# Performance work log

Hardware: AMD Instinct MI355X
Metric: run time of the kernel (lower is better)

The kernel has to match this reference:

```python
import jax, jax.numpy as jnp
import numpy as np

NUM_HEADS = 16

def _split_heads(x, H):
    B, S, D = x.shape
    return x.reshape(B, S, H, D // H).transpose(0, 2, 1, 3)  # [B,H,S,hd]

def _merge_heads(x):
    B, H, S, hd = x.shape
    return x.transpose(0, 2, 1, 3).reshape(B, S, H * hd)

def setup_inputs() -> dict:
    key = jax.random.key(0)
    k1, k2, k3, k4 = jax.random.split(key, 4)
    B, S, D = 2, 2048, 1024
    return {
        "visual_features": jax.random.normal(k1, (B, S, D), dtype=jnp.float32),
        "transaction_features": jax.random.normal(k2, (B, S, D), dtype=jnp.float32),
        "W_qkv": jax.random.normal(k3, (D, 3 * D), dtype=jnp.float32) * (1.0 / np.sqrt(D)),
        "W_out": jax.random.normal(k4, (D, D), dtype=jnp.float32) * (1.0 / np.sqrt(D)),
    }

def reference(visual_features, transaction_features, W_qkv, W_out):
    H = NUM_HEADS
    D = visual_features.shape[-1]
    scale = (D // H) ** -0.5

    v_q, v_k, v_v = [_split_heads(t, H) for t in jnp.split(visual_features @ W_qkv, 3, axis=-1)]
    t_q, t_k, t_v = [_split_heads(t, H) for t in jnp.split(transaction_features @ W_qkv, 3, axis=-1)]

    # visual queries attend to transaction keys/values (dropout = identity at eval)
    v2t = jax.nn.softmax(jnp.einsum('bhqd,bhkd->bhqk', v_q, t_k) * scale, axis=-1)
    t2v = jax.nn.softmax(jnp.einsum('bhqd,bhkd->bhqk', t_q, v_k) * scale, axis=-1)

    v2t_out = _merge_heads(jnp.einsum('bhqk,bhkd->bhqd', v2t, t_v))
    t2v_out = _merge_heads(jnp.einsum('bhqk,bhkd->bhqd', t2v, v_v))

    return (v2t_out + t2v_out) @ W_out
```

## Files before the change

kernel.cpp:

```cpp
#include <hip/hip_runtime.h>


typedef short  frag8 __attribute__((ext_vector_type(8)));
typedef float  f32x4 __attribute__((ext_vector_type(4)));

union F8 { frag8 f; uint2 u2[2]; unsigned u[4]; };

#define MFMA16(a,b,c) __builtin_amdgcn_mfma_f32_16x16x32_bf16((a),(b),(c),0,0,0)

__device__ __forceinline__ unsigned short f2bf(float f) {
  unsigned u = __builtin_bit_cast(unsigned, f);
  return (unsigned short)((u + 0x7fffu + ((u >> 16) & 1u)) >> 16);
}
__device__ __forceinline__ float bf2f(unsigned short s) {
  unsigned u = ((unsigned)s) << 16;
  return __builtin_bit_cast(float, u);
}
__device__ __forceinline__ unsigned pkbf(float lo, float hi) {
  unsigned r;
  asm("v_cvt_pk_bf16_f32 %0, %1, %2" : "=v"(r) : "v"(lo), "v"(hi));
  return r;
}

__global__ __launch_bounds__(256) void k_prep(
    const float* __restrict__ vis, const float* __restrict__ trn,
    const float* __restrict__ Wqkv, const float* __restrict__ Wout,
    unsigned short* __restrict__ Abf, unsigned short* __restrict__ Wqb,
    unsigned short* __restrict__ Wob)
{
  size_t i8 = ((size_t)blockIdx.x * 256 + threadIdx.x) * 8;
  const float* src;
  unsigned short* dst;
  if (i8 < 8388608) {
    src = (i8 < 4194304) ? vis + i8 : trn + (i8 - 4194304);
    dst = Abf + i8;
  } else if (i8 < 11534336) {
    size_t o = i8 - 8388608;  src = Wqkv + o; dst = Wqb + o;
  } else {
    size_t o = i8 - 11534336; src = Wout + o; dst = Wob + o;
  }
  float4 u = *(const float4*)src;
  float4 v = *(const float4*)(src + 4);
  uint4 w;
  w.x = pkbf(u.x, u.y); w.y = pkbf(u.z, u.w);
  w.z = pkbf(v.x, v.y); w.w = pkbf(v.z, v.w);
  *(uint4*)dst = w;
}

__global__ __launch_bounds__(256) void k_gemm_qkv_b(
    const unsigned short* __restrict__ Abf, const unsigned short* __restrict__ Wqb,
    unsigned short* __restrict__ qkv)
{
  __shared__ unsigned short As_[128 * 32];
  __shared__ unsigned short Bs[128 * 40];
  const int tid  = threadIdx.x;
  const int lane = tid & 63, wv = tid >> 6;
  const int lm = lane & 15, lg = lane >> 4;
  const int nt = blockIdx.x, mt = blockIdx.y;
  const int wr = (wv >> 1) * 64, wc = (wv & 1) * 64;

  f32x4 acc[4][4] = {};

  const unsigned short* agp =
      Abf + (size_t)(mt * 128 + wv * 32 + (lane >> 2)) * 1024 + (lane & 3) * 8;
  const int bn = (tid & 63) * 2, bk = (tid >> 6) * 8;

  for (int kt = 0; kt < 32; ++kt) {
    __syncthreads();
    {
      __builtin_amdgcn_global_load_lds(
          (const __attribute__((address_space(1))) void*)(agp + kt * 32),
          (__attribute__((address_space(3))) void*)&As_[wv * 1024], 16, 0, 0);
      __builtin_amdgcn_global_load_lds(
          (const __attribute__((address_space(1))) void*)(agp + 16 * 1024 + kt * 32),
          (__attribute__((address_space(3))) void*)&As_[wv * 1024 + 512], 16, 0, 0);
    }
    {
      const unsigned short* bp = Wqb + (size_t)(kt * 32 + bk) * 3072 + nt * 128 + bn;
      frag8 q0, q1;
#pragma unroll
      for (int i = 0; i < 8; ++i) {
        ushort2 t = *(const ushort2*)(bp + (size_t)i * 3072);
        q0[i] = (short)t.x; q1[i] = (short)t.y;
      }
      *(frag8*)&Bs[(bn)     * 40 + bk] = q0;
      *(frag8*)&Bs[(bn + 1) * 40 + bk] = q1;
    }
    __syncthreads();
    frag8 af[4], bfr[4];
#pragma unroll
    for (int mi = 0; mi < 4; ++mi)
      af[mi] = *(const frag8*)&As_[(wr + mi * 16 + lm) * 32 + lg * 8];
#pragma unroll
    for (int ni = 0; ni < 4; ++ni)
      bfr[ni] = *(const frag8*)&Bs[(wc + ni * 16 + lm) * 40 + lg * 8];
#pragma unroll
    for (int mi = 0; mi < 4; ++mi)
#pragma unroll
      for (int ni = 0; ni < 4; ++ni)
        acc[mi][ni] = MFMA16(af[mi], bfr[ni], acc[mi][ni]);
  }

#pragma unroll
  for (int mi = 0; mi < 4; ++mi)
#pragma unroll
    for (int ni = 0; ni < 4; ++ni)
#pragma unroll
      for (int r = 0; r < 4; ++r) {
        int row = mt * 128 + wr + mi * 16 + lg * 4 + r;
        int col = nt * 128 + wc + ni * 16 + lm;
        qkv[(size_t)row * 3072 + col] = f2bf(acc[mi][ni][r]);
      }
}

__global__ __launch_bounds__(256) void k_vt(
    const unsigned short* __restrict__ qkv, unsigned short* __restrict__ Vt)
{
  __shared__ unsigned short L[64 * 72];
  const int tid = threadIdx.x;
  const int sblk = blockIdx.x;
  const int by = blockIdx.y;
  const int src = by >> 4, h = by & 15;
  {
    int sl = tid >> 2, dc = tid & 3;
    const unsigned short* gp =
        qkv + (size_t)(src * 2048 + sblk * 64 + sl) * 3072 + 2048 + h * 64 + dc * 16;
    *(frag8*)&L[sl * 72 + dc * 16]     = *(const frag8*)gp;
    *(frag8*)&L[sl * 72 + dc * 16 + 8] = *(const frag8*)(gp + 8);
  }
  __syncthreads();
  int d = tid >> 2, sc = tid & 3;
  unsigned wbuf[8];
#pragma unroll
  for (int j = 0; j < 8; ++j) {
    unsigned lo = L[(sc * 16 + 2 * j)     * 72 + d];
    unsigned hi = L[(sc * 16 + 2 * j + 1) * 72 + d];
    wbuf[j] = lo | (hi << 16);
  }
  unsigned short* op =
      Vt + ((size_t)(src * 16 + h) * 64 + d) * 2048 + sblk * 64 + sc * 16;
  *(uint4*)op       = *(uint4*)&wbuf[0];
  *(uint4*)(op + 8) = *(uint4*)&wbuf[4];
}

__global__ __launch_bounds__(256) void k_attn(
    const unsigned short* __restrict__ qkv, const unsigned short* __restrict__ Vt,
    unsigned short* __restrict__ Opart, float* __restrict__ lpart)
{
  __shared__ unsigned short Ks[2][32 * 72];
  __shared__ unsigned short Vs[2][8 * 272];
  const int tid  = threadIdx.x;
  const int lane = tid & 63, wv = tid >> 6;
  const int lm = lane & 15, lg = lane >> 4;
  const int qt = blockIdx.x, comb = blockIdx.y;
  const int dir = comb >> 5, bb = (comb >> 4) & 1, h = comb & 15;
  const int half = blockIdx.z;
  const int NT = 32, kt0 = half * 32;
  const int qbase  = (dir ? 4096 : 0) + bb * 2048;
  const int kvbase = (dir ? 0 : 4096) + bb * 2048;
  const int qcol = h * 64, kcol = 1024 + h * 64;

  const float QS = 0.125f * 1.44269504f;
  frag8 qf[2][2];
#pragma unroll
  for (int mi = 0; mi < 2; ++mi)
#pragma unroll
    for (int kb = 0; kb < 2; ++kb) {
      frag8 t = *(const frag8*)&qkv[
          (size_t)(qbase + qt * 128 + wv * 32 + mi * 16 + lm) * 3072 +
          qcol + kb * 32 + lg * 8];
#pragma unroll
      for (int j = 0; j < 8; ++j)
        t[j] = (short)f2bf(bf2f((unsigned short)t[j]) * QS);
      qf[mi][kb] = t;
    }

  f32x4 acc[2][4] = {};
  float lr[2] = {0.0f, 0.0f};

  const int skv = tid >> 3, sd = (tid & 7) * 8;
  const int vd = tid >> 2, vc = tid & 3;
  const unsigned short* __restrict__ kp =
      qkv + (size_t)(kvbase + skv) * 3072 + kcol + sd;
  const unsigned short* __restrict__ vtp =
      Vt + ((size_t)((kvbase >> 11) * 16 + h) * 64 + vd) * 2048 + vc * 8;

  frag8 Rk, Rv;

#define LOAD_R(kt_) do {                                                   \
    Rk = *(const frag8*)(kp + (size_t)(kt_) * (32 * 3072));                \
    Rv = *(const frag8*)(vtp + (size_t)(kt_) * 32);                        \
  } while (0)

#define WRITE_R(s_) do {                                                   \
    *(frag8*)&Ks[s_][skv * 72 + sd] = Rk;                                  \
    F8 tv_; tv_.f = Rv;                                                    \
    *(uint2*)&Vs[s_][(2 * vc) * 272 + vd * 4]     = tv_.u2[0];             \
    *(uint2*)&Vs[s_][(2 * vc + 1) * 272 + vd * 4] = tv_.u2[1];             \
  } while (0)

  LOAD_R(kt0);
  WRITE_R(0);
  LOAD_R(kt0 + 1);

  for (int i = 0; i < NT; ++i) {
    __syncthreads();
    if (i < NT - 1) WRITE_R((i + 1) & 1);
    if (i < NT - 2) LOAD_R(kt0 + i + 2);
    const int s = i & 1;

    frag8 kf[2][2];
#pragma unroll
    for (int t = 0; t < 2; ++t)
#pragma unroll
      for (int kb = 0; kb < 2; ++kb)
        kf[t][kb] = *(const frag8*)&Ks[s][(t * 16 + lm) * 72 + kb * 32 + lg * 8];
    f32x4 st[2][2] = {};
#pragma unroll
    for (int mi = 0; mi < 2; ++mi)
#pragma unroll
      for (int t = 0; t < 2; ++t)
#pragma unroll
        for (int kb = 0; kb < 2; ++kb)
          st[mi][t] = MFMA16(kf[t][kb], qf[mi][kb], st[mi][t]);

    frag8 pa[2];
#pragma unroll
    for (int mi = 0; mi < 2; ++mi) {
      f32x4 a = st[mi][0], b = st[mi][1];
      float p[8];
#pragma unroll
      for (int r = 0; r < 4; ++r) p[r]     = exp2f(a[r]);
#pragma unroll
      for (int r = 0; r < 4; ++r) p[4 + r] = exp2f(b[r]);
      lr[mi] += ((p[0] + p[1]) + (p[2] + p[3])) +
                ((p[4] + p[5]) + (p[6] + p[7]));
      F8 pk_;
      pk_.u[0] = pkbf(p[0], p[1]); pk_.u[1] = pkbf(p[2], p[3]);
      pk_.u[2] = pkbf(p[4], p[5]); pk_.u[3] = pkbf(p[6], p[7]);
      pa[mi] = pk_.f;
    }

    frag8 vb[4];
#pragma unroll
    for (int di = 0; di < 4; ++di) {
      F8 t;
      t.u2[0] = *(const uint2*)&Vs[s][lg * 272 + (di * 16 + lm) * 4];
      t.u2[1] = *(const uint2*)&Vs[s][(4 + lg) * 272 + (di * 16 + lm) * 4];
      vb[di] = t.f;
    }
#pragma unroll
    for (int mi = 0; mi < 2; ++mi)
#pragma unroll
      for (int di = 0; di < 4; ++di)
        acc[mi][di] = MFMA16(pa[mi], vb[di], acc[mi][di]);
  }

#undef LOAD_R
#undef WRITE_R

#pragma unroll
  for (int mi = 0; mi < 2; ++mi) {
    float l = lr[mi];
    l += __shfl_xor(l, 16);
    l += __shfl_xor(l, 32);
    int rowb = bb * 2048 + qt * 128 + wv * 32 + mi * 16;
    if (lane < 16)
      lpart[(size_t)(half * 2 + dir) * 65536 + h * 4096 + rowb + lane] = l;
#pragma unroll
    for (int r = 0; r < 4; ++r) {
      int row = rowb + lg * 4 + r;
#pragma unroll
      for (int di = 0; di < 4; ++di) {
        int col = h * 64 + di * 16 + lm;
        Opart[((size_t)(half * 2 + dir) * 4096 + row) * 1024 + col] =
            f2bf(acc[mi][di][r]);
      }
    }
  }
}

__global__ __launch_bounds__(256) void k_combine(
    const unsigned short* __restrict__ Op, const float* __restrict__ lp,
    unsigned short* __restrict__ a0, unsigned short* __restrict__ a1)
{
  int g   = blockIdx.x * 256 + threadIdx.x;
  int col = (g & 255) << 2;
  int row = (g >> 8) & 4095;
  int dir = g >> 20;
  int h   = col >> 6;
  float l = lp[(size_t)dir * 65536 + h * 4096 + row] +
            lp[(size_t)(2 + dir) * 65536 + h * 4096 + row];
  float inv = 1.0f / l;
  const unsigned short* pu = &Op[((size_t)dir * 4096 + row) * 1024 + col];
  const unsigned short* pv = &Op[((size_t)(2 + dir) * 4096 + row) * 1024 + col];
  uint2 w;
  w.x = pkbf((bf2f(pu[0]) + bf2f(pv[0])) * inv, (bf2f(pu[1]) + bf2f(pv[1])) * inv);
  w.y = pkbf((bf2f(pu[2]) + bf2f(pv[2])) * inv, (bf2f(pu[3]) + bf2f(pv[3])) * inv);
  unsigned short* dst = dir ? a1 : a0;
  *(uint2*)&dst[(size_t)row * 1024 + col] = w;
}

__global__ __launch_bounds__(256) void k_gemm_out_b(
    const unsigned short* __restrict__ x0, const unsigned short* __restrict__ x1,
    const unsigned short* __restrict__ Wob, float* __restrict__ out)
{
  __shared__ unsigned short As[128 * 40];
  __shared__ unsigned short Bs[128 * 40];
  const int tid  = threadIdx.x;
  const int lane = tid & 63, wv = tid >> 6;
  const int lm = lane & 15, lg = lane >> 4;
  const int nt = blockIdx.x, mt = blockIdx.y;
  const int wr = (wv >> 1) * 64, wc = (wv & 1) * 64;

  f32x4 acc[4][4] = {};

  const int am = tid >> 1, akq = (tid & 1) * 16;
  const int arow = mt * 128 + am;
  const unsigned short* __restrict__ a0p = x0 + (size_t)arow * 1024;
  const unsigned short* __restrict__ a1p = x1 + (size_t)arow * 1024;
  const int bn = (tid & 63) * 2, bk = (tid >> 6) * 8;

  for (int kt = 0; kt < 32; ++kt) {
    __syncthreads();
    {
      frag8 u0 = *(const frag8*)(a0p + kt * 32 + akq);
      frag8 u1 = *(const frag8*)(a0p + kt * 32 + akq + 8);
      frag8 w0 = *(const frag8*)(a1p + kt * 32 + akq);
      frag8 w1 = *(const frag8*)(a1p + kt * 32 + akq + 8);
      frag8 p0, p1;
#pragma unroll
      for (int j = 0; j < 8; ++j) {
        p0[j] = (short)f2bf(bf2f((unsigned short)u0[j]) + bf2f((unsigned short)w0[j]));
        p1[j] = (short)f2bf(bf2f((unsigned short)u1[j]) + bf2f((unsigned short)w1[j]));
      }
      *(frag8*)&As[am * 40 + akq]     = p0;
      *(frag8*)&As[am * 40 + akq + 8] = p1;
    }
    {
      const unsigned short* bp = Wob + (size_t)(kt * 32 + bk) * 1024 + nt * 128 + bn;
      frag8 q0, q1;
#pragma unroll
      for (int i = 0; i < 8; ++i) {
        ushort2 t = *(const ushort2*)(bp + (size_t)i * 1024);
        q0[i] = (short)t.x; q1[i] = (short)t.y;
      }
      *(frag8*)&Bs[(bn)     * 40 + bk] = q0;
      *(frag8*)&Bs[(bn + 1) * 40 + bk] = q1;
    }
    __syncthreads();
    frag8 af[4], bfr[4];
#pragma unroll
    for (int mi = 0; mi < 4; ++mi)
      af[mi] = *(const frag8*)&As[(wr + mi * 16 + lm) * 40 + lg * 8];
#pragma unroll
    for (int ni = 0; ni < 4; ++ni)
      bfr[ni] = *(const frag8*)&Bs[(wc + ni * 16 + lm) * 40 + lg * 8];
#pragma unroll
    for (int mi = 0; mi < 4; ++mi)
#pragma unroll
      for (int ni = 0; ni < 4; ++ni)
        acc[mi][ni] = MFMA16(af[mi], bfr[ni], acc[mi][ni]);
  }

#pragma unroll
  for (int mi = 0; mi < 4; ++mi)
#pragma unroll
    for (int ni = 0; ni < 4; ++ni)
#pragma unroll
      for (int r = 0; r < 4; ++r) {
        int row = mt * 128 + wr + mi * 16 + lg * 4 + r;
        int col = nt * 128 + wc + ni * 16 + lm;
        out[(size_t)row * 1024 + col] = acc[mi][ni][r];
      }
}

extern "C" void kernel_launch(void* const* d_in, const int* in_sizes, int n_in,
                              void* d_out, int out_size, void* d_ws, size_t ws_size,
                              hipStream_t stream)
{
  const float* vis  = (const float*)d_in[0];
  const float* trn  = (const float*)d_in[1];
  const float* Wqkv = (const float*)d_in[2];
  const float* Wout = (const float*)d_in[3];
  float* out = (float*)d_out;

  char* base = (char*)d_ws;
  unsigned short* qkv = (unsigned short*)base;
  unsigned short* a0  = (unsigned short*)(base + 50331648UL);
  unsigned short* a1  = a0 + 4194304;
  unsigned short* Vt  = (unsigned short*)(base + 67108864UL);
  unsigned short* Wob = (unsigned short*)(base + 83886080UL);
  float*          lp  = (float*)(base + 85983232UL);
  unsigned short* Abf = (unsigned short*)(base + 87031808UL);
  unsigned short* Wqb = Abf + 8388608;
  unsigned short* Op  = (unsigned short*)(base + 87031808UL);

  k_prep     <<<6144, 256, 0, stream>>>(vis, trn, Wqkv, Wout, Abf, Wqb, Wob);
  k_gemm_qkv_b<<<dim3(24, 64), 256, 0, stream>>>(Abf, Wqb, qkv);
  k_vt       <<<dim3(32, 64), 256, 0, stream>>>(qkv, Vt);
  k_attn     <<<dim3(16, 64, 2), 256, 0, stream>>>(qkv, Vt, Op, lp);
  k_combine  <<<8192, 256, 0, stream>>>(Op, lp, a0, a1);
  k_gemm_out_b<<<dim3(8, 32), 256, 0, stream>>>(a0, a1, Wob, out);
}
```

Before: 268.4 us.

## Pre-transpose weights to N-major bf16 and stream B tiles via global_load_lds

Adds a k_wt kernel that converts W_qkv and W_out to bf16 and transposes them to [N][K] layout through shared memory. Both GEMMs can then load B tiles with direct global-to-LDS 16-byte loads instead of strided 2-element gathers and register transposes. The softmax exp2f calls are also replaced with raw v_exp_f32 inline asm, which skips the library's range handling. The cost is two extra small launches per call, and the exp change relies on inputs staying in the range the hardware instruction handles.

Result: faster. 243.7 us (-9.2%).

```diff
diff --git a/kernel.cpp b/kernel.cpp
--- a/kernel.cpp
+++ b/kernel.cpp
@@ -21,38 +21,63 @@
   asm("v_cvt_pk_bf16_f32 %0, %1, %2" : "=v"(r) : "v"(lo), "v"(hi));
   return r;
 }
+__device__ __forceinline__ float fexp2(float x) {
+  float r;
+  asm("v_exp_f32 %0, %1" : "=v"(r) : "v"(x));
+  return r;
+}
 
 __global__ __launch_bounds__(256) void k_prep(
     const float* __restrict__ vis, const float* __restrict__ trn,
-    const float* __restrict__ Wqkv, const float* __restrict__ Wout,
-    unsigned short* __restrict__ Abf, unsigned short* __restrict__ Wqb,
-    unsigned short* __restrict__ Wob)
+    unsigned short* __restrict__ Abf)
 {
   size_t i8 = ((size_t)blockIdx.x * 256 + threadIdx.x) * 8;
-  const float* src;
-  unsigned short* dst;
-  if (i8 < 8388608) {
-    src = (i8 < 4194304) ? vis + i8 : trn + (i8 - 4194304);
-    dst = Abf + i8;
-  } else if (i8 < 11534336) {
-    size_t o = i8 - 8388608;  src = Wqkv + o; dst = Wqb + o;
-  } else {
-    size_t o = i8 - 11534336; src = Wout + o; dst = Wob + o;
-  }
+  const float* src = (i8 < 4194304) ? vis + i8 : trn + (i8 - 4194304);
   float4 u = *(const float4*)src;
   float4 v = *(const float4*)(src + 4);
   uint4 w;
   w.x = pkbf(u.x, u.y); w.y = pkbf(u.z, u.w);
   w.z = pkbf(v.x, v.y); w.w = pkbf(v.z, v.w);
-  *(uint4*)dst = w;
+  *(uint4*)(Abf + i8) = w;
+}
+
+__global__ __launch_bounds__(256) void k_wt(
+    const float* __restrict__ W, unsigned short* __restrict__ Wt, int N)
+{
+  __shared__ unsigned short L[64 * 72];
+  const int tid = threadIdx.x;
+  const int n0 = blockIdx.x * 64, k0 = blockIdx.y * 64;
+  {
+    int kr = tid >> 2, c4 = (tid & 3) * 16;
+    const float* gp = W + (size_t)(k0 + kr) * N + n0 + c4;
+    float4 u0 = *(const float4*)gp,       u1 = *(const float4*)(gp + 4);
+    float4 u2 = *(const float4*)(gp + 8), u3 = *(const float4*)(gp + 12);
+    unsigned* lw = (unsigned*)&L[kr * 72 + c4];
+    lw[0] = pkbf(u0.x, u0.y); lw[1] = pkbf(u0.z, u0.w);
+    lw[2] = pkbf(u1.x, u1.y); lw[3] = pkbf(u1.z, u1.w);
+    lw[4] = pkbf(u2.x, u2.y); lw[5] = pkbf(u2.z, u2.w);
+    lw[6] = pkbf(u3.x, u3.y); lw[7] = pkbf(u3.z, u3.w);
+  }
+  __syncthreads();
+  int nr = tid >> 2, kc = (tid & 3) * 16;
+  unsigned wb[8];
+#pragma unroll
+  for (int j = 0; j < 8; ++j) {
+    unsigned lo = L[(kc + 2 * j)     * 72 + nr];
+    unsigned hi = L[(kc + 2 * j + 1) * 72 + nr];
+    wb[j] = lo | (hi << 16);
+  }
+  unsigned short* op = Wt + (size_t)(n0 + nr) * 1024 + k0 + kc;
+  *(uint4*)op       = *(uint4*)&wb[0];
+  *(uint4*)(op + 8) = *(uint4*)&wb[4];
 }
 
 __global__ __launch_bounds__(256) void k_gemm_qkv_b(
-    const unsigned short* __restrict__ Abf, const unsigned short* __restrict__ Wqb,
+    const unsigned short* __restrict__ Abf, const unsigned short* __restrict__ WqbT,
     unsigned short* __restrict__ qkv)
 {
   __shared__ unsigned short As_[128 * 32];
-  __shared__ unsigned short Bs[128 * 40];
+  __shared__ unsigned short Bs_[128 * 32];
   const int tid  = threadIdx.x;
   const int lane = tid & 63, wv = tid >> 6;
   const int lm = lane & 15, lg = lane >> 4;
@@ -63,29 +88,23 @@
 
   const unsigned short* agp =
       Abf + (size_t)(mt * 128 + wv * 32 + (lane >> 2)) * 1024 + (lane & 3) * 8;
-  const int bn = (tid & 63) * 2, bk = (tid >> 6) * 8;
+  const unsigned short* bgp =
+      WqbT + (size_t)(nt * 128 + wv * 32 + (lane >> 2)) * 1024 + (lane & 3) * 8;
 
   for (int kt = 0; kt < 32; ++kt) {
     __syncthreads();
-    {
-      __builtin_amdgcn_global_load_lds(
-          (const __attribute__((address_space(1))) void*)(agp + kt * 32),
-          (__attribute__((address_space(3))) void*)&As_[wv * 1024], 16, 0, 0);
-      __builtin_amdgcn_global_load_lds(
-          (const __attribute__((address_space(1))) void*)(agp + 16 * 1024 + kt * 32),
-          (__attribute__((address_space(3))) void*)&As_[wv * 1024 + 512], 16, 0, 0);
-    }
-    {
-      const unsigned short* bp = Wqb + (size_t)(kt * 32 + bk) * 3072 + nt * 128 + bn;
-      frag8 q0, q1;
-#pragma unroll
-      for (int i = 0; i < 8; ++i) {
-        ushort2 t = *(const ushort2*)(bp + (size_t)i * 3072);
-        q0[i] = (short)t.x; q1[i] = (short)t.y;
-      }
-      *(frag8*)&Bs[(bn)     * 40 + bk] = q0;
-      *(frag8*)&Bs[(bn + 1) * 40 + bk] = q1;
-    }
+    __builtin_amdgcn_global_load_lds(
+        (const __attribute__((address_space(1))) void*)(agp + kt * 32),
+        (__attribute__((address_space(3))) void*)&As_[wv * 1024], 16, 0, 0);
+    __builtin_amdgcn_global_load_lds(
+        (const __attribute__((address_space(1))) void*)(agp + 16 * 1024 + kt * 32),
+        (__attribute__((address_space(3))) void*)&As_[wv * 1024 + 512], 16, 0, 0);
+    __builtin_amdgcn_global_load_lds(
+        (const __attribute__((address_space(1))) void*)(bgp + kt * 32),
+        (__attribute__((address_space(3))) void*)&Bs_[wv * 1024], 16, 0, 0);
+    __builtin_amdgcn_global_load_lds(
+        (const __attribute__((address_space(1))) void*)(bgp + 16 * 1024 + kt * 32),
+        (__attribute__((address_space(3))) void*)&Bs_[wv * 1024 + 512], 16, 0, 0);
     __syncthreads();
     frag8 af[4], bfr[4];
 #pragma unroll
@@ -93,7 +112,7 @@
       af[mi] = *(const frag8*)&As_[(wr + mi * 16 + lm) * 32 + lg * 8];
 #pragma unroll
     for (int ni = 0; ni < 4; ++ni)
-      bfr[ni] = *(const frag8*)&Bs[(wc + ni * 16 + lm) * 40 + lg * 8];
+      bfr[ni] = *(const frag8*)&Bs_[(wc + ni * 16 + lm) * 32 + lg * 8];
 #pragma unroll
     for (int mi = 0; mi < 4; ++mi)
 #pragma unroll
@@ -230,9 +249,9 @@
       f32x4 a = st[mi][0], b = st[mi][1];
       float p[8];
 #pragma unroll
-      for (int r = 0; r < 4; ++r) p[r]     = exp2f(a[r]);
-#pragma unroll
-      for (int r = 0; r < 4; ++r) p[4 + r] = exp2f(b[r]);
+      for (int r = 0; r < 4; ++r) p[r]     = fexp2(a[r]);
+#pragma unroll
+      for (int r = 0; r < 4; ++r) p[4 + r] = fexp2(b[r]);
       lr[mi] += ((p[0] + p[1]) + (p[2] + p[3])) +
                 ((p[4] + p[5]) + (p[6] + p[7]));
       F8 pk_;
@@ -303,10 +322,10 @@
 
 __global__ __launch_bounds__(256) void k_gemm_out_b(
     const unsigned short* __restrict__ x0, const unsigned short* __restrict__ x1,
-    const unsigned short* __restrict__ Wob, float* __restrict__ out)
+    const unsigned short* __restrict__ WobT, float* __restrict__ out)
 {
   __shared__ unsigned short As[128 * 40];
-  __shared__ unsigned short Bs[128 * 40];
+  __shared__ unsigned short Bs_[128 * 32];
   const int tid  = threadIdx.x;
   const int lane = tid & 63, wv = tid >> 6;
   const int lm = lane & 15, lg = lane >> 4;
@@ -319,10 +338,17 @@
   const int arow = mt * 128 + am;
   const unsigned short* __restrict__ a0p = x0 + (size_t)arow * 1024;
   const unsigned short* __restrict__ a1p = x1 + (size_t)arow * 1024;
-  const int bn = (tid & 63) * 2, bk = (tid >> 6) * 8;
+  const unsigned short* bgp =
+      WobT + (size_t)(nt * 128 + wv * 32 + (lane >> 2)) * 1024 + (lane & 3) * 8;
 
   for (int kt = 0; kt < 32; ++kt) {
     __syncthreads();
+    __builtin_amdgcn_global_load_lds(
+        (const __attribute__((address_space(1))) void*)(bgp + kt * 32),
+        (__attribute__((address_space(3))) void*)&Bs_[wv * 1024], 16, 0, 0);
+    __builtin_amdgcn_global_load_lds(
+        (const __attribute__((address_space(1))) void*)(bgp + 16 * 1024 + kt * 32),
+        (__attribute__((address_space(3))) void*)&Bs_[wv * 1024 + 512], 16, 0, 0);
     {
       frag8 u0 = *(const frag8*)(a0p + kt * 32 + akq);
       frag8 u1 = *(const frag8*)(a0p + kt * 32 + akq + 8);
@@ -337,17 +363,6 @@
       *(frag8*)&As[am * 40 + akq]     = p0;
       *(frag8*)&As[am * 40 + akq + 8] = p1;
     }
-    {
-      const unsigned short* bp = Wob + (size_t)(kt * 32 + bk) * 1024 + nt * 128 + bn;
-      frag8 q0, q1;
-#pragma unroll
-      for (int i = 0; i < 8; ++i) {
-        ushort2 t = *(const ushort2*)(bp + (size_t)i * 1024);
-        q0[i] = (short)t.x; q1[i] = (short)t.y;
-      }
-      *(frag8*)&Bs[(bn)     * 40 + bk] = q0;
-      *(frag8*)&Bs[(bn + 1) * 40 + bk] = q1;
-    }
     __syncthreads();
     frag8 af[4], bfr[4];
 #pragma unroll
@@ -355,7 +370,7 @@
       af[mi] = *(const frag8*)&As[(wr + mi * 16 + lm) * 40 + lg * 8];
 #pragma unroll
     for (int ni = 0; ni < 4; ++ni)
-      bfr[ni] = *(const frag8*)&Bs[(wc + ni * 16 + lm) * 40 + lg * 8];
+      bfr[ni] = *(const frag8*)&Bs_[(wc + ni * 16 + lm) * 32 + lg * 8];
 #pragma unroll
     for (int mi = 0; mi < 4; ++mi)
 #pragma unroll
@@ -386,20 +401,22 @@
   float* out = (float*)d_out;
 
   char* base = (char*)d_ws;
-  unsigned short* qkv = (unsigned short*)base;
-  unsigned short* a0  = (unsigned short*)(base + 50331648UL);
-  unsigned short* a1  = a0 + 4194304;
-  unsigned short* Vt  = (unsigned short*)(base + 67108864UL);
-  unsigned short* Wob = (unsigned short*)(base + 83886080UL);
-  float*          lp  = (float*)(base + 85983232UL);
-  unsigned short* Abf = (unsigned short*)(base + 87031808UL);
-  unsigned short* Wqb = Abf + 8388608;
-  unsigned short* Op  = (unsigned short*)(base + 87031808UL);
-
-  k_prep     <<<6144, 256, 0, stream>>>(vis, trn, Wqkv, Wout, Abf, Wqb, Wob);
-  k_gemm_qkv_b<<<dim3(24, 64), 256, 0, stream>>>(Abf, Wqb, qkv);
-  k_vt       <<<dim3(32, 64), 256, 0, stream>>>(qkv, Vt);
-  k_attn     <<<dim3(16, 64, 2), 256, 0, stream>>>(qkv, Vt, Op, lp);
-  k_combine  <<<8192, 256, 0, stream>>>(Op, lp, a0, a1);
-  k_gemm_out_b<<<dim3(8, 32), 256, 0, stream>>>(a0, a1, Wob, out);
-}
+  unsigned short* qkv  = (unsigned short*)base;
+  unsigned short* a0   = (unsigned short*)(base + 50331648UL);
+  unsigned short* a1   = a0 + 4194304;
+  unsigned short* Vt   = (unsigned short*)(base + 67108864UL);
+  unsigned short* WobT = (unsigned short*)(base + 83886080UL);
+  float*          lp   = (float*)(base + 85983232UL);
+  unsigned short* Abf  = (unsigned short*)(base + 87031808UL);
+  unsigned short* WqbT = Abf + 8388608;
+  unsigned short* Op   = (unsigned short*)(base + 87031808UL);
+
+  k_prep      <<<4096, 256, 0, stream>>>(vis, trn, Abf);
+  k_wt        <<<dim3(48, 16), 256, 0, stream>>>(Wqkv, WqbT, 3072);
+  k_wt        <<<dim3(16, 16), 256, 0, stream>>>(Wout, WobT, 1024);
+  k_gemm_qkv_b<<<dim3(24, 64), 256, 0, stream>>>(Abf, WqbT, qkv);
+  k_vt        <<<dim3(32, 64), 256, 0, stream>>>(qkv, Vt);
+  k_attn      <<<dim3(16, 64, 2), 256, 0, stream>>>(qkv, Vt, Op, lp);
+  k_combine   <<<8192, 256, 0, stream>>>(Op, lp, a0, a1);
+  k_gemm_out_b<<<dim3(8, 32), 256, 0, stream>>>(a0, a1, WobT, out);
+}
```
